# Kernel optimization log

Measured on AMD Instinct MI355X. Metric: run time of the kernel, lower is better.

## Reference

```python
import jax, jax.numpy as jnp
import numpy as np

DIM_HEAD = 64
HEADS = 8

def rotate_half(x):
    x1, x2 = jnp.split(x, 2, axis=-1)
    return jnp.concatenate((-x2, x1), axis=-1)

def apply_rope(pos, t):
    # pos: [N, d] broadcast against t: [B, H, N, d]
    return t * jnp.cos(pos) + rotate_half(t) * jnp.sin(pos)

def setup_inputs() -> dict:
    key = jax.random.key(0)
    k1, k2, k3, k4 = jax.random.split(key, 4)
    B, N, C = 2, 4096, 512
    inner = HEADS * DIM_HEAD
    x = jax.random.normal(k1, (B, N, C), dtype=jnp.float32)
    pos_emb = jax.random.normal(k2, (N, DIM_HEAD), dtype=jnp.float32)
    w_qkv = jax.random.normal(k3, (C, inner * 3), dtype=jnp.float32) * (1.0 / np.sqrt(C))
    w_out = jax.random.normal(k4, (inner, C), dtype=jnp.float32) * (1.0 / np.sqrt(inner))
    b_out = jnp.zeros((C,), dtype=jnp.float32)
    return {"x": x, "pos_emb": pos_emb, "w_qkv": w_qkv, "w_out": w_out, "b_out": b_out}

def reference(x, pos_emb, w_qkv, w_out, b_out):
    B, N, C = x.shape
    scale = DIM_HEAD ** -0.5
    qkv = x @ w_qkv  # [B, N, 3*inner]
    q, k, v = jnp.split(qkv, 3, axis=-1)
    def to_heads(t):
        return t.reshape(B, N, HEADS, DIM_HEAD).transpose(0, 2, 1, 3)  # [B,H,N,d]
    q, k, v = to_heads(q), to_heads(k), to_heads(v)
    q = apply_rope(pos_emb, q)
    k = apply_rope(pos_emb, k)
    dots = jnp.einsum('bhid,bhjd->bhij', q, k) * scale  # [B,H,N,N]
    attn = jax.nn.softmax(dots, axis=-1)
    out = jnp.einsum('bhij,bhjd->bhid', attn, v)
    out = out.transpose(0, 2, 1, 3).reshape(B, N, HEADS * DIM_HEAD)
    return out @ w_out + b_out
```

## Files before the change

### kernel.cpp

```cpp
#include <hip/hip_runtime.h>


typedef float    floatx4 __attribute__((ext_vector_type(4)));
typedef _Float16 half8   __attribute__((ext_vector_type(8)));
typedef _Float16 half4   __attribute__((ext_vector_type(4)));

__device__ __forceinline__ float fast_exp2(float x) {
#if __has_builtin(__builtin_amdgcn_exp2f)
  return __builtin_amdgcn_exp2f(x);
#else
  float r;
  asm("v_exp_f32 %0, %1" : "=v"(r) : "v"(x));
  return r;
#endif
}

__device__ __forceinline__ void async16(const void* g, void* l) {
  __builtin_amdgcn_global_load_lds(
      (const __attribute__((address_space(1))) void*)g,
      (__attribute__((address_space(3))) void*)l, 16, 0, 0);
}

__global__ __launch_bounds__(256) void prep(
    const float* __restrict__ X, const float* __restrict__ pos,
    const float* __restrict__ Wqkv, const float* __restrict__ Wout,
    _Float16* __restrict__ A2, float2* __restrict__ CSSN,
    _Float16* __restrict__ B2qkv, _Float16* __restrict__ B2out) {
  __shared__ float tile[64][65];
  const int bid = blockIdx.x, t = threadIdx.x;
  if (bid < 4096) {
    const int i = (bid * 256 + t) * 4;
    const float4 v = *(const float4*)(X + i);
    half4 h;
    h[0] = (_Float16)v.x; h[1] = (_Float16)v.y;
    h[2] = (_Float16)v.z; h[3] = (_Float16)v.w;
    *(half4*)(A2 + i) = h;
  } else if (bid < 5120) {
    const int i = (bid - 4096) * 256 + t;
    const float p = pos[i];
    CSSN[i] = make_float2(__cosf(p), __sinf(p));
  } else {
    const float* W; _Float16* B2T; int Ncols, bx, by;
    if (bid < 5312) { const int idx = bid - 5120; bx = idx % 24; by = idx / 24;
                      W = Wqkv; B2T = B2qkv; Ncols = 1536; }
    else            { const int idx = bid - 5312; bx = idx % 8;  by = idx / 8;
                      W = Wout; B2T = B2out; Ncols = 512; }
    const int k0 = by * 64, n0 = bx * 64;
    const int lane = t & 63, w = t >> 6;
#pragma unroll 4
    for (int i = 0; i < 16; ++i) {
      const int k = w * 16 + i;
      tile[k][lane] = W[(size_t)(k0 + k) * Ncols + n0 + lane];
    }
    __syncthreads();
#pragma unroll 4
    for (int i = 0; i < 16; ++i) {
      const int n = w * 16 + i;
      B2T[(size_t)(n0 + n) * 512 + k0 + lane] = (_Float16)tile[lane][n];
    }
  }
}

__global__ __launch_bounds__(256) void gemm_qkv_rope(
    const _Float16* __restrict__ A2, const _Float16* __restrict__ B2T,
    const float2* __restrict__ CSSN,
    _Float16* __restrict__ Qb, _Float16* __restrict__ Kb,
    _Float16* __restrict__ VT) {
  __shared__ __align__(16) _Float16 ldsA[128 * 64];
  __shared__ __align__(16) _Float16 ldsB[128 * 64];
  __shared__ __align__(16) _Float16 qk_lds[4][16][72];
  const int t = threadIdx.x, w = t >> 6, l = t & 63;
  const int lo = l & 15, hi = l >> 4, sw = lo & 7;
  const int m0 = blockIdx.y << 7, n0 = blockIdx.x << 7;

  const int strow = w * 8 + (l >> 3);
  const int schunk = (l & 7) ^ ((l >> 3) & 7);
  const _Float16* gA = A2 + (size_t)(m0 + strow) * 512 + schunk * 8;
  const _Float16* gB = B2T + (size_t)(n0 + strow) * 512 + schunk * 8;
  _Float16* lA = ldsA + w * 512 + l * 8;
  _Float16* lB = ldsB + w * 512 + l * 8;

  const int mw = (w >> 1) * 64, nw = (w & 1) * 64;

  floatx4 acc[4][4];
#pragma unroll
  for (int mt = 0; mt < 4; ++mt)
#pragma unroll
    for (int nt = 0; nt < 4; ++nt) acc[mt][nt] = (floatx4){0.f, 0.f, 0.f, 0.f};

  for (int ks = 0; ks < 8; ++ks) {
    const int kk = ks * 64;
    __syncthreads();
#pragma unroll
    for (int i = 0; i < 4; ++i) {
      async16(gA + (size_t)i * 32 * 512 + kk, lA + i * 2048);
      async16(gB + (size_t)i * 32 * 512 + kk, lB + i * 2048);
    }
    __syncthreads();
#pragma unroll
    for (int kc = 0; kc < 2; ++kc) {
      const int slot = ((hi + 4 * kc) ^ sw) * 8;
      half8 af[4], bf[4];
#pragma unroll
      for (int mt = 0; mt < 4; ++mt)
        af[mt] = *(const half8*)(ldsA + (mw + mt * 16 + lo) * 64 + slot);
#pragma unroll
      for (int nt = 0; nt < 4; ++nt)
        bf[nt] = *(const half8*)(ldsB + (nw + nt * 16 + lo) * 64 + slot);
#pragma unroll
      for (int mt = 0; mt < 4; ++mt)
#pragma unroll
        for (int nt = 0; nt < 4; ++nt)
          acc[mt][nt] = __builtin_amdgcn_mfma_f32_16x16x32_f16(
              af[mt], bf[nt], acc[mt][nt], 0, 0, 0);
    }
  }

  const int bx = blockIdx.x;
  const int kind = bx >> 2;
  const int h = ((bx & 3) << 1) | (nw >> 6);
  if (kind == 2) {
#pragma unroll
    for (int mt = 0; mt < 4; ++mt) {
      const int rowb = m0 + mw + mt * 16 + hi * 4;
      const int b = rowb >> 12, nn = rowb & 4095;
#pragma unroll
      for (int nt = 0; nt < 4; ++nt) {
        const int dd = nt * 16 + lo;
        half4 v4;
#pragma unroll
        for (int r = 0; r < 4; ++r) v4[r] = (_Float16)acc[mt][nt][r];
        *(half4*)(VT + ((size_t)((b * 8 + h) * 64 + dd)) * 4096 + nn) = v4;
      }
    }
  } else {
    _Float16* Db = (kind == 0) ? Qb : Kb;
    const float sc = (kind == 0) ? 0.125f * 1.44269504f : 1.0f;
    _Float16 (*qt_)[72] = qk_lds[w];
#pragma unroll
    for (int mt = 0; mt < 4; ++mt) {
#pragma unroll
      for (int r = 0; r < 4; ++r) {
        const int row = m0 + mw + mt * 16 + hi * 4 + r;
        const int nn = row & 4095;
        const float2* cp = CSSN + (size_t)nn * 64 + lo;
#pragma unroll
        for (int nt = 0; nt < 4; ++nt) {
          const float2 cs = cp[nt * 16];
          const float x0 = acc[mt][nt][r];
          const float xp = acc[mt][nt ^ 2][r];
          const float rot = (nt & 2) ? xp : -xp;
          qt_[hi * 4 + r][nt * 16 + lo] = (_Float16)((x0 * cs.x + rot * cs.y) * sc);
        }
      }
#pragma unroll
      for (int pass = 0; pass < 2; ++pass) {
        const int rr = pass * 8 + (l >> 3);
        const int dcol = (l & 7) * 8;
        const half8 v = *(const half8*)&qt_[rr][dcol];
        const int row = m0 + mw + mt * 16 + rr;
        const int b = row >> 12, nn = row & 4095;
        *(half8*)(Db + ((size_t)((b * 8 + h) * 4096 + nn)) * 64 + dcol) = v;
      }
    }
  }
}

__global__ __launch_bounds__(256) void gemm_out_f16(
    const _Float16* __restrict__ A2, const _Float16* __restrict__ B2T,
    const float* __restrict__ bias, float* __restrict__ C) {
  __shared__ __align__(16) _Float16 ldsA[128 * 64];
  __shared__ __align__(16) _Float16 ldsB[64 * 64];
  const int t = threadIdx.x, w = t >> 6, l = t & 63;
  const int lo = l & 15, hi = l >> 4, sw = lo & 7;
  const int m0 = blockIdx.y << 7, n0 = blockIdx.x << 6;

  const int strow = w * 8 + (l >> 3);
  const int schunk = (l & 7) ^ ((l >> 3) & 7);
  const _Float16* gA = A2 + (size_t)(m0 + strow) * 512 + schunk * 8;
  const _Float16* gB = B2T + (size_t)(n0 + strow) * 512 + schunk * 8;
  _Float16* lA = ldsA + w * 512 + l * 8;
  _Float16* lB = ldsB + w * 512 + l * 8;

  const int mw = (w >> 1) * 64, nw = (w & 1) * 32;

  floatx4 acc[4][2];
#pragma unroll
  for (int mt = 0; mt < 4; ++mt)
#pragma unroll
    for (int nt = 0; nt < 2; ++nt) acc[mt][nt] = (floatx4){0.f, 0.f, 0.f, 0.f};

  for (int ks = 0; ks < 8; ++ks) {
    const int kk = ks * 64;
    __syncthreads();
#pragma unroll
    for (int i = 0; i < 4; ++i)
      async16(gA + (size_t)i * 32 * 512 + kk, lA + i * 2048);
#pragma unroll
    for (int i = 0; i < 2; ++i)
      async16(gB + (size_t)i * 32 * 512 + kk, lB + i * 2048);
    __syncthreads();
#pragma unroll
    for (int kc = 0; kc < 2; ++kc) {
      const int slot = ((hi + 4 * kc) ^ sw) * 8;
      half8 af[4], bf[2];
#pragma unroll
      for (int mt = 0; mt < 4; ++mt)
        af[mt] = *(const half8*)(ldsA + (mw + mt * 16 + lo) * 64 + slot);
#pragma unroll
      for (int nt = 0; nt < 2; ++nt)
        bf[nt] = *(const half8*)(ldsB + (nw + nt * 16 + lo) * 64 + slot);
#pragma unroll
      for (int mt = 0; mt < 4; ++mt)
#pragma unroll
        for (int nt = 0; nt < 2; ++nt)
          acc[mt][nt] = __builtin_amdgcn_mfma_f32_16x16x32_f16(
              af[mt], bf[nt], acc[mt][nt], 0, 0, 0);
    }
  }
#pragma unroll
  for (int mt = 0; mt < 4; ++mt)
#pragma unroll
    for (int r = 0; r < 4; ++r) {
      const int row = m0 + mw + mt * 16 + hi * 4 + r;
#pragma unroll
      for (int nt = 0; nt < 2; ++nt) {
        const int col = n0 + nw + nt * 16 + lo;
        C[(size_t)row * 512 + col] = acc[mt][nt][r] + bias[col];
      }
    }
}

__global__ __launch_bounds__(256, 4) void flash_attn(
    const _Float16* __restrict__ Qb, const _Float16* __restrict__ Kb,
    const _Float16* __restrict__ VT, _Float16* __restrict__ Opart,
    float* __restrict__ lpart) {
  __shared__ __align__(16) _Float16 ldsK[64 * 64];
  __shared__ __align__(16) _Float16 ldsV[64 * 64];
  const int t = threadIdx.x;
  const int w = t >> 6, l = t & 63;
  const int lo = l & 15, hi = l >> 4;
  const int sw = lo & 7;
  const int bh = blockIdx.y, qt = blockIdx.x, sp = blockIdx.z;

  const int srow = l >> 3;
  const int scol = (l & 7) ^ srow;
  const int goffK = srow * 64 + scol * 8;
  const size_t goffV = (size_t)srow * 4096 + scol * 8;
  const int ldst = l * 8;

  const _Float16* Qrow = Qb + ((size_t)bh * 4096 + qt * 128 + w * 32 + lo) * 64;
  half8 qf[2][2];
  qf[0][0] = *(const half8*)(Qrow + hi * 8);
  qf[0][1] = *(const half8*)(Qrow + hi * 8 + 32);
  qf[1][0] = *(const half8*)(Qrow + 16 * 64 + hi * 8);
  qf[1][1] = *(const half8*)(Qrow + 16 * 64 + hi * 8 + 32);

  floatx4 acc[2][4];
  float l_s[2] = {0.f, 0.f};
#pragma unroll
  for (int g = 0; g < 2; ++g)
#pragma unroll
    for (int dt = 0; dt < 4; ++dt) acc[g][dt] = (floatx4){0.f, 0.f, 0.f, 0.f};

  const _Float16* Kt = Kb + (size_t)bh * 4096 * 64;
  const _Float16* Vt = VT + (size_t)bh * 64 * 4096;

  for (int tt = sp * 32; tt < sp * 32 + 32; ++tt) {
    __syncthreads();
    {
      const _Float16* gK = Kt + (size_t)tt * 4096;
      const _Float16* gV = Vt + tt * 64;
      const int k0 = w * 2;
      async16(gK + (size_t)k0 * 512 + goffK,       ldsK + k0 * 512 + ldst);
      async16(gK + (size_t)(k0 + 1) * 512 + goffK, ldsK + (k0 + 1) * 512 + ldst);
      async16(gV + (size_t)k0 * 32768 + goffV,       ldsV + k0 * 512 + ldst);
      async16(gV + (size_t)(k0 + 1) * 32768 + goffV, ldsV + (k0 + 1) * 512 + ldst);
    }
    __syncthreads();

    floatx4 st[2][4];
#pragma unroll
    for (int jt = 0; jt < 4; ++jt) {
      const _Float16* kr = ldsK + (jt * 16 + lo) * 64;
      const half8 kf0 = *(const half8*)(kr + ((hi ^ sw) * 8));
      const half8 kf1 = *(const half8*)(kr + (((hi + 4) ^ sw) * 8));
#pragma unroll
      for (int g = 0; g < 2; ++g) {
        floatx4 z = (floatx4){0.f, 0.f, 0.f, 0.f};
        z = __builtin_amdgcn_mfma_f32_16x16x32_f16(kf0, qf[g][0], z, 0, 0, 0);
        z = __builtin_amdgcn_mfma_f32_16x16x32_f16(kf1, qf[g][1], z, 0, 0, 0);
        st[g][jt] = z;
      }
    }

    half4 pf[2][4];
#pragma unroll
    for (int g = 0; g < 2; ++g)
#pragma unroll
      for (int jt = 0; jt < 4; ++jt) {
        const float e0 = fast_exp2(st[g][jt][0]);
        const float e1 = fast_exp2(st[g][jt][1]);
        const float e2 = fast_exp2(st[g][jt][2]);
        const float e3 = fast_exp2(st[g][jt][3]);
        l_s[g] += (e0 + e1) + (e2 + e3);
        uint2 u;
        u.x = __builtin_bit_cast(unsigned, __builtin_amdgcn_cvt_pkrtz(e0, e1));
        u.y = __builtin_bit_cast(unsigned, __builtin_amdgcn_cvt_pkrtz(e2, e3));
        pf[g][jt] = __builtin_bit_cast(half4, u);
      }

#pragma unroll
    for (int dt = 0; dt < 4; ++dt) {
      half4 vf[4];
#pragma unroll
      for (int jt = 0; jt < 4; ++jt)
        vf[jt] = *(const half4*)(ldsV + (dt * 16 + lo) * 64 +
                                 (((jt * 2 + (hi >> 1)) ^ sw) * 8) + (hi & 1) * 4);
#pragma unroll
      for (int g = 0; g < 2; ++g)
#pragma unroll
        for (int jt = 0; jt < 4; ++jt)
          acc[g][dt] = __builtin_amdgcn_mfma_f32_16x16x16f16(
              pf[g][jt], vf[jt], acc[g][dt], 0, 0, 0);
    }
  }

  _Float16* obase = Opart + ((size_t)(sp * 16 + bh)) * 4096 * 64;
  float*    lbase = lpart + ((size_t)(sp * 16 + bh)) * 4096;
#pragma unroll
  for (int g = 0; g < 2; ++g) {
    float v = l_s[g];
    v += __shfl_xor(v, 16);
    v += __shfl_xor(v, 32);
    if (hi == 0)
      lbase[qt * 128 + w * 32 + g * 16 + lo] = v;
#pragma unroll
    for (int r = 0; r < 4; ++r) {
      const int q = qt * 128 + w * 32 + g * 16 + hi * 4 + r;
#pragma unroll
      for (int dt = 0; dt < 4; ++dt)
        obase[(size_t)q * 64 + dt * 16 + lo] = (_Float16)acc[g][dt][r];
    }
  }
}

__global__ __launch_bounds__(256) void combine_splits(
    const _Float16* __restrict__ Opart, const float* __restrict__ lpart,
    _Float16* __restrict__ O2) {
  const int idx = blockIdx.x * 256 + threadIdx.x;
  const int d0 = (idx & 15) * 4;
  const int q  = (idx >> 4) & 4095;
  const int bh = idx >> 16;
  const int b = bh >> 3, h = bh & 7;
  const half4 a0 = *(const half4*)(Opart + ((size_t)bh * 4096 + q) * 64 + d0);
  const half4 a1 = *(const half4*)(Opart + ((size_t)(16 + bh) * 4096 + q) * 64 + d0);
  const float lsum = lpart[(size_t)bh * 4096 + q] +
                     lpart[(size_t)(16 + bh) * 4096 + q];
  const float inv = 1.f / lsum;
  half4 o;
#pragma unroll
  for (int i = 0; i < 4; ++i)
    o[i] = (_Float16)(((float)a0[i] + (float)a1[i]) * inv);
  *(half4*)(O2 + ((size_t)(b * 4096 + q)) * 512 + h * 64 + d0) = o;
}

extern "C" void kernel_launch(void* const* d_in, const int* in_sizes, int n_in,
                              void* d_out, int out_size, void* d_ws, size_t ws_size,
                              hipStream_t stream) {
  const float* x     = (const float*)d_in[0];
  const float* pos   = (const float*)d_in[1];
  const float* w_qkv = (const float*)d_in[2];
  const float* w_out = (const float*)d_in[3];
  const float* b_out = (const float*)d_in[4];
  float* out = (float*)d_out;

  char* ws = (char*)d_ws;
  if (ws_size < (size_t)56 * 1024 * 1024) return;

  const size_t MB = 1024 * 1024;
  _Float16* A2x   = (_Float16*)ws;
  _Float16* O2    = (_Float16*)ws;
  _Float16* B2qkv = (_Float16*)(ws + 8 * MB);
  float2*   CSSN  = (float2*)(ws + 11 * MB);
  _Float16* Qb    = (_Float16*)(ws + 13 * MB);
  _Float16* Kb    = (_Float16*)(ws + 21 * MB);
  _Float16* VT    = (_Float16*)(ws + 29 * MB);
  _Float16* Opart = (_Float16*)(ws + 37 * MB);
  float*    lpart = (float*)(ws + 53 * MB);
  _Float16* B2out = (_Float16*)(ws + 54 * MB);

  prep<<<5376, 256, 0, stream>>>(x, pos, w_qkv, w_out, A2x, CSSN, B2qkv, B2out);
  gemm_qkv_rope<<<dim3(12, 64), 256, 0, stream>>>(A2x, B2qkv, CSSN, Qb, Kb, VT);
  flash_attn<<<dim3(32, 16, 2), 256, 0, stream>>>(Qb, Kb, VT, Opart, lpart);
  combine_splits<<<4096, 256, 0, stream>>>(Opart, lpart, O2);
  gemm_out_f16<<<dim3(8, 64), 256, 0, stream>>>(O2, B2out, b_out, out);
}
```

Before: 210.8 us.

## Double-buffer K/V tiles and use 16x16x32 MFMA for PV via permlane swap

```diff
diff --git a/kernel.cpp b/kernel.cpp
--- a/kernel.cpp
+++ b/kernel.cpp
@@ -4,6 +4,7 @@
 typedef float    floatx4 __attribute__((ext_vector_type(4)));
 typedef _Float16 half8   __attribute__((ext_vector_type(8)));
 typedef _Float16 half4   __attribute__((ext_vector_type(4)));
+typedef unsigned uintx4  __attribute__((ext_vector_type(4)));
 
 __device__ __forceinline__ float fast_exp2(float x) {
 #if __has_builtin(__builtin_amdgcn_exp2f)
@@ -19,6 +20,10 @@
   __builtin_amdgcn_global_load_lds(
       (const __attribute__((address_space(1))) void*)g,
       (__attribute__((address_space(3))) void*)l, 16, 0, 0);
+}
+
+__device__ __forceinline__ void pl32swap(unsigned& a, unsigned& b) {
+  asm("v_permlane32_swap_b32 %0, %1" : "+v"(a), "+v"(b));
 }
 
 __global__ __launch_bounds__(256) void prep(
@@ -235,12 +240,14 @@
     const _Float16* __restrict__ Qb, const _Float16* __restrict__ Kb,
     const _Float16* __restrict__ VT, _Float16* __restrict__ Opart,
     float* __restrict__ lpart) {
-  __shared__ __align__(16) _Float16 ldsK[64 * 64];
-  __shared__ __align__(16) _Float16 ldsV[64 * 64];
+  __shared__ __align__(16) _Float16 ldsK[2][64 * 64];
+  __shared__ __align__(16) _Float16 ldsV[2][64 * 64];
   const int t = threadIdx.x;
   const int w = t >> 6, l = t & 63;
   const int lo = l & 15, hi = l >> 4;
   const int sw = lo & 7;
+  const int lop = (lo & 3) | ((lo & 4) << 1) | ((lo & 8) >> 1);
+  const int swk = lop & 7;
   const int bh = blockIdx.y, qt = blockIdx.x, sp = blockIdx.z;
 
   const int srow = l >> 3;
@@ -266,25 +273,37 @@
   const _Float16* Kt = Kb + (size_t)bh * 4096 * 64;
   const _Float16* Vt = VT + (size_t)bh * 64 * 4096;
 
-  for (int tt = sp * 32; tt < sp * 32 + 32; ++tt) {
-    __syncthreads();
-    {
-      const _Float16* gK = Kt + (size_t)tt * 4096;
-      const _Float16* gV = Vt + tt * 64;
-      const int k0 = w * 2;
-      async16(gK + (size_t)k0 * 512 + goffK,       ldsK + k0 * 512 + ldst);
-      async16(gK + (size_t)(k0 + 1) * 512 + goffK, ldsK + (k0 + 1) * 512 + ldst);
-      async16(gV + (size_t)k0 * 32768 + goffV,       ldsV + k0 * 512 + ldst);
-      async16(gV + (size_t)(k0 + 1) * 32768 + goffV, ldsV + (k0 + 1) * 512 + ldst);
-    }
-    __syncthreads();
+  auto stage = [&](int buf, int tt) {
+    const _Float16* gK = Kt + (size_t)tt * 4096;
+    const _Float16* gV = Vt + tt * 64;
+    _Float16* dK = &ldsK[buf][0];
+    _Float16* dV = &ldsV[buf][0];
+    const int k0 = w * 2;
+    async16(gK + (size_t)k0 * 512 + goffK,         dK + k0 * 512 + ldst);
+    async16(gK + (size_t)(k0 + 1) * 512 + goffK,   dK + (k0 + 1) * 512 + ldst);
+    async16(gV + (size_t)k0 * 32768 + goffV,       dV + k0 * 512 + ldst);
+    async16(gV + (size_t)(k0 + 1) * 32768 + goffV, dV + (k0 + 1) * 512 + ldst);
+  };
+
+  stage(0, sp * 32);
+  for (int it = 0; it < 32; ++it) {
+    const int cur = it & 1;
+    if (it != 31) {
+      stage(cur ^ 1, sp * 32 + it + 1);
+      asm volatile("s_waitcnt vmcnt(4)" ::: "memory");
+    } else {
+      asm volatile("s_waitcnt vmcnt(0)" ::: "memory");
+    }
+    __builtin_amdgcn_s_barrier();
+    const _Float16* ldsKc = &ldsK[cur][0];
+    const _Float16* ldsVc = &ldsV[cur][0];
 
     floatx4 st[2][4];
 #pragma unroll
     for (int jt = 0; jt < 4; ++jt) {
-      const _Float16* kr = ldsK + (jt * 16 + lo) * 64;
-      const half8 kf0 = *(const half8*)(kr + ((hi ^ sw) * 8));
-      const half8 kf1 = *(const half8*)(kr + (((hi + 4) ^ sw) * 8));
+      const _Float16* kr = ldsKc + (jt * 16 + lop) * 64;
+      const half8 kf0 = *(const half8*)(kr + ((hi ^ swk) * 8));
+      const half8 kf1 = *(const half8*)(kr + (((hi + 4) ^ swk) * 8));
 #pragma unroll
       for (int g = 0; g < 2; ++g) {
         floatx4 z = (floatx4){0.f, 0.f, 0.f, 0.f};
@@ -294,7 +313,7 @@
       }
     }
 
-    half4 pf[2][4];
+    unsigned pfx[2][4], pfy[2][4];
 #pragma unroll
     for (int g = 0; g < 2; ++g)
 #pragma unroll
@@ -304,26 +323,37 @@
         const float e2 = fast_exp2(st[g][jt][2]);
         const float e3 = fast_exp2(st[g][jt][3]);
         l_s[g] += (e0 + e1) + (e2 + e3);
-        uint2 u;
-        u.x = __builtin_bit_cast(unsigned, __builtin_amdgcn_cvt_pkrtz(e0, e1));
-        u.y = __builtin_bit_cast(unsigned, __builtin_amdgcn_cvt_pkrtz(e2, e3));
-        pf[g][jt] = __builtin_bit_cast(half4, u);
+        pfx[g][jt] = __builtin_bit_cast(unsigned, __builtin_amdgcn_cvt_pkrtz(e0, e1));
+        pfy[g][jt] = __builtin_bit_cast(unsigned, __builtin_amdgcn_cvt_pkrtz(e2, e3));
+      }
+
+    half8 paf[2][2];
+#pragma unroll
+    for (int g = 0; g < 2; ++g)
+#pragma unroll
+      for (int j2 = 0; j2 < 2; ++j2) {
+        pl32swap(pfx[g][2 * j2], pfx[g][2 * j2 + 1]);
+        pl32swap(pfy[g][2 * j2], pfy[g][2 * j2 + 1]);
+        uintx4 u;
+        u[0] = pfx[g][2 * j2];     u[1] = pfy[g][2 * j2];
+        u[2] = pfx[g][2 * j2 + 1]; u[3] = pfy[g][2 * j2 + 1];
+        paf[g][j2] = __builtin_bit_cast(half8, u);
       }
 
 #pragma unroll
     for (int dt = 0; dt < 4; ++dt) {
-      half4 vf[4];
-#pragma unroll
-      for (int jt = 0; jt < 4; ++jt)
-        vf[jt] = *(const half4*)(ldsV + (dt * 16 + lo) * 64 +
-                                 (((jt * 2 + (hi >> 1)) ^ sw) * 8) + (hi & 1) * 4);
-#pragma unroll
-      for (int g = 0; g < 2; ++g)
-#pragma unroll
-        for (int jt = 0; jt < 4; ++jt)
-          acc[g][dt] = __builtin_amdgcn_mfma_f32_16x16x16f16(
-              pf[g][jt], vf[jt], acc[g][dt], 0, 0, 0);
-    }
+      const _Float16* vrow = ldsVc + (dt * 16 + lo) * 64;
+      const half8 vf0 = *(const half8*)(vrow + ((hi ^ sw) * 8));
+      const half8 vf1 = *(const half8*)(vrow + (((4 + hi) ^ sw) * 8));
+#pragma unroll
+      for (int g = 0; g < 2; ++g) {
+        acc[g][dt] = __builtin_amdgcn_mfma_f32_16x16x32_f16(
+            paf[g][0], vf0, acc[g][dt], 0, 0, 0);
+        acc[g][dt] = __builtin_amdgcn_mfma_f32_16x16x32_f16(
+            paf[g][1], vf1, acc[g][dt], 0, 0, 0);
+      }
+    }
+    __builtin_amdgcn_s_barrier();
   }
 
   _Float16* obase = Opart + ((size_t)(sp * 16 + bh)) * 4096 * 64;
```

Result: no change. 208.9 us (-0.9%).
